# Optimization experiments

Hardware: AMD Instinct MI355X
Metric: run time of the kernel (lower is better)

## Reference

```python
import jax, jax.numpy as jnp
from jax import lax
import numpy as np

GRIDS = [40, 36, 24, 16, 12]
STRIDES = [4, 8, 16, 32, 64]
SCORE_THR = 0.3
MASK_THR = 0.5
UPDATE_THR = 0.05
SIGMA = 2.0
NMS_PRE = 500
MAX_PER_IMG = 30
E = 128            # ins_out_channels -> kernel_out_channels
HF = WF = 128      # seg feature map; upsampled_size_out = 4*HF = 512
IMG_H = IMG_W = 512
ORI_H = ORI_W = 512

# per-candidate stride, matching the cumsum-based fill in get_seg_single
STRIDE_PER_CELL = np.repeat(np.array(STRIDES, np.float32), [g * g for g in GRIDS])  # [3872]


def setup_inputs() -> dict:
    key = jax.random.key(0)
    ks = jax.random.split(key, 11)
    d = {}
    for i, g in enumerate(GRIDS):
        d[f"cate{i}"] = jax.random.uniform(ks[i], (1, g, g, 1), jnp.float32)
        d[f"kern{i}"] = jax.random.normal(ks[5 + i], (1, E, g, g), jnp.float32)
    d["seg_pred"] = jax.random.normal(ks[10], (1, E, HF, WF), jnp.float32)
    return d


def _forward_scores_and_masks(cates, kerns, seg_pred):
    # flatten all FPN levels, exactly mirroring view(-1,C)/permute(1,2,0).view(-1,E)
    scores = jnp.concatenate([c[0].reshape(-1) for c in cates])                 # [M]
    kernels = jnp.concatenate([k[0].transpose(1, 2, 0).reshape(-1, E) for k in kerns])  # [M,E]
    strides = jnp.asarray(STRIDE_PER_CELL)
    valid = scores > SCORE_THR                                                  # score_thr filter (as mask)

    # dynamic 1x1 conv over mask features == channel contraction
    seg_preds = jax.nn.sigmoid(jnp.einsum('me,ehw->mhw', kernels, seg_pred[0]))  # [M,HF,WF]
    seg_masks = seg_preds > MASK_THR
    sum_masks = seg_masks.sum((1, 2)).astype(jnp.float32)
    keep = valid & (sum_masks > strides)
    seg_scores = (seg_preds * seg_masks).sum((1, 2)) / jnp.maximum(sum_masks, 1.0)
    cscores = jnp.where(keep, scores * seg_scores, 0.0)

    # descending sort + truncate to nms_pre (dropped candidates carry score 0)
    top_scores, top_idx = lax.top_k(cscores, NMS_PRE)
    masks_k = seg_masks[top_idx].reshape(NMS_PRE, -1).astype(jnp.float32)       # [N,HW]
    sm = sum_masks[top_idx]

    # matrix NMS (single foreground class -> label matrix = triu of ones)
    inter = masks_k @ masks_k.T                                                 # [N,N]
    union = sm[None, :] + sm[:, None] - inter
    iou = jnp.triu(inter / jnp.maximum(union, 1.0), k=1)
    comp = iou.max(0)                              # max IoU with any higher-scored mask
    decay = jnp.exp(-SIGMA * (iou ** 2 - comp[:, None] ** 2))
    decay_coeff = decay.min(0)
    nms_scores = top_scores * decay_coeff
    nms_scores = jnp.where(nms_scores >= UPDATE_THR, nms_scores, 0.0)           # update_thr filter

    final_scores, fidx = lax.top_k(nms_scores, MAX_PER_IMG)
    sel = top_idx[fidx]
    sel_preds = seg_preds[sel]                                                  # [K,HF,WF]
    up = jax.image.resize(sel_preds, (MAX_PER_IMG, HF * 4, WF * 4), 'bilinear')  # align_corners=False
    up = up[:, :IMG_H, :IMG_W]
    up = jax.image.resize(up, (MAX_PER_IMG, ORI_H, ORI_W), 'bilinear')
    return final_scores, up


def reference(cate0, cate1, cate2, cate3, cate4,
              kern0, kern1, kern2, kern3, kern4, seg_pred):
    cates = [cate0, cate1, cate2, cate3, cate4]
    kerns = [kern0, kern1, kern2, kern3, kern4]
    final_scores, up = _forward_scores_and_masks(cates, kerns, seg_pred)
    seg_label = up > MASK_THR                                                   # [K,H,W]
    vis = final_scores > SCORE_THR                                              # vis_inds in forward()

    # masks_to_boxes, vectorized; invalid/empty rows zeroed (fixed-size output)
    any_x = seg_label.any(1)                                                    # [K,W]
    any_y = seg_label.any(2)                                                    # [K,H]
    xs = jnp.arange(ORI_W)
    ys = jnp.arange(ORI_H)
    xmin = jnp.min(jnp.where(any_x, xs, ORI_W), axis=1)
    xmax = jnp.max(jnp.where(any_x, xs, -1), axis=1)
    ymin = jnp.min(jnp.where(any_y, ys, ORI_H), axis=1)
    ymax = jnp.max(jnp.where(any_y, ys, -1), axis=1)
    boxes = jnp.stack([xmin, ymin, xmax, ymax], -1).astype(jnp.float32)         # [K,4]
    boxes = jnp.where(vis[:, None], boxes, 0.0)
    return boxes, final_scores, vis.astype(jnp.float32)
```

## Files before the change

kernel.cpp:

```cpp
#include <hip/hip_runtime.h>
#include <math.h>

#define M_CELLS 3872
#define M_PAD   3968
#define NPIX    16384

typedef _Float16 half8 __attribute__((ext_vector_type(8)));
typedef float f32x4 __attribute__((ext_vector_type(4)));

#define GL2LDS(g, l) __builtin_amdgcn_global_load_lds( \
    (const __attribute__((address_space(1))) unsigned int*)(g), \
    (__attribute__((address_space(3))) unsigned int*)(l), 16, 0, 0)

static constexpr size_t ALN(size_t x){ return (x + 255) & ~(size_t)255; }

static constexpr size_t F_KF   = 0;
static constexpr size_t F_SC   = F_KF + (size_t)M_CELLS*128*4;
static constexpr size_t F_SM   = F_SC + (size_t)M_CELLS*4;
static constexpr size_t F_CS   = F_SM + (size_t)M_CELLS*4;
static constexpr size_t F_BIT  = F_CS + (size_t)M_CELLS*4;
static constexpr size_t F_SPP  = F_BIT + (size_t)M_CELLS*256*8;
static constexpr size_t F_TIDX = F_SPP + (size_t)64*M_CELLS*4;
static constexpr size_t F_TSC  = F_TIDX + 512*4;
static constexpr size_t F_SMT  = F_TSC + 512*4;
static constexpr size_t F_IOU  = F_SMT + 512*4;
static constexpr size_t F_COMP = F_IOU + (size_t)500*500*4;
static constexpr size_t F_NMS  = F_COMP + 512*4;
static constexpr size_t F_SEL  = F_NMS + 512*4;
static constexpr size_t F_SELP = F_SEL + 32*4;
static constexpr size_t F_GAX  = ALN(F_SELP + (size_t)30*NPIX*4);
static constexpr size_t F_GAY  = F_GAX + 30*512*4;
static constexpr size_t F_KEYS = ALN(F_GAY + 30*512*4);
static constexpr size_t WS_FB  = F_KEYS + 4096*8;

static constexpr size_t B_KF   = 0;
static constexpr size_t B_AFR  = ALN(B_KF  + (size_t)M_PAD*128*4);
static constexpr size_t B_BFR  = ALN(B_AFR + (size_t)31*4096*16);
static constexpr size_t B_SC   = ALN(B_BFR + (size_t)128*4096*16);
static constexpr size_t B_SM   = ALN(B_SC + (size_t)M_PAD*4);
static constexpr size_t B_CS   = ALN(B_SM + (size_t)M_PAD*4);
static constexpr size_t B_BIT  = ALN(B_CS + (size_t)M_PAD*4);
static constexpr size_t B_SPP  = ALN(B_BIT + (size_t)M_PAD*256*8);
static constexpr size_t B_TIDX = ALN(B_SPP + (size_t)128*M_PAD*4);
static constexpr size_t B_TSC  = ALN(B_TIDX + 512*4);
static constexpr size_t B_SMT  = ALN(B_TSC + 512*4);
static constexpr size_t B_IOU  = ALN(B_SMT + 512*4);
static constexpr size_t B_COMP = ALN(B_IOU + (size_t)500*500*4);
static constexpr size_t B_NMS  = ALN(B_COMP + 512*4);
static constexpr size_t B_SEL  = ALN(B_NMS + 512*4);
static constexpr size_t B_SELP = ALN(B_SEL + 32*4);
static constexpr size_t B_GAX  = ALN(B_SELP + (size_t)30*NPIX*4);
static constexpr size_t B_GAY  = B_GAX + 30*512*4;
static constexpr size_t B_CMAP = ALN(B_GAY + 30*512*4);
static constexpr size_t B_RMAP = B_CMAP + 4096*4;
static constexpr size_t B_VCNT = B_RMAP + 4096*4;
static constexpr size_t B_KEYS = ALN(B_VCNT + 64*4);
static constexpr size_t B_AF30 = ALN(B_KEYS + 4096*8);
static constexpr size_t WS_MFMA = B_AF30 + 8*128*16;

__global__ __launch_bounds__(256) void k0a_gather(
    const float* __restrict__ c0,const float* __restrict__ c1,const float* __restrict__ c2,
    const float* __restrict__ c3,const float* __restrict__ c4,
    const float* __restrict__ w0,const float* __restrict__ w1,const float* __restrict__ w2,
    const float* __restrict__ w3,const float* __restrict__ w4,
    float* __restrict__ kf, float* __restrict__ scores) {
  const int lvl = blockIdx.y;
  const int Gs[5]   = {1600,1296,576,256,144};
  const int offs[5] = {0,1600,2896,3472,3728};
  const int G = Gs[lvl], off = offs[lvl];
  const float* kl = (lvl==0)?w0:(lvl==1)?w1:(lvl==2)?w2:(lvl==3)?w3:w4;
  const float* cl = (lvl==0)?c0:(lvl==1)?c1:(lvl==2)?c2:(lvl==3)?c3:c4;
  int t = blockIdx.x*256 + threadIdx.x;
  if (t >= G*128) return;
  int e = t / G, c = t - e*G;
  kf[(size_t)(off+c)*128 + e] = kl[t];
  if (e == 0) scores[off+c] = cl[c];
}

__global__ __launch_bounds__(1024) void k_compact(const float* __restrict__ scores,
                                                  int* __restrict__ cmap, int* __restrict__ rmap,
                                                  int* __restrict__ vcnt) {
  __shared__ int tsum[1024];
  int tid = threadIdx.x;
  int base = tid*4;
  int f[4]; int s = 0;
  #pragma unroll
  for (int j=0;j<4;j++) {
    int c = base+j;
    f[j] = (c < M_CELLS && scores[c] > 0.3f) ? 1 : 0;
    s += f[j];
  }
  tsum[tid] = s;
  __syncthreads();
  for (int off=1; off<1024; off<<=1) {
    int v = (tid >= off) ? tsum[tid-off] : 0;
    __syncthreads();
    tsum[tid] += v;
    __syncthreads();
  }
  int run = tsum[tid] - s;
  #pragma unroll
  for (int j=0;j<4;j++) {
    int c = base+j;
    if (c < M_CELLS) {
      if (f[j]) { cmap[run] = c; rmap[c] = run; run++; }
      else rmap[c] = -1;
    }
  }
  if (tid == 1023) vcnt[0] = tsum[1023];
}

__global__ __launch_bounds__(256) void k0b_afrag(const float* __restrict__ kf,
                                                 const int* __restrict__ cmap,
                                                 const int* __restrict__ vcnt,
                                                 _Float16* __restrict__ Af) {
  int P = blockIdx.x*256 + threadIdx.x;
  int mblock = P >> 12;
  int r  = P & 4095;
  int sub = r >> 9, pc = r & 511;
  int ks = sub >> 1, h = sub & 1;
  int mn = pc >> 6, ln = pc & 63;
  int mcomp = mblock*128 + mn*16 + (ln & 15);
  int kb = ks*32 + (ln >> 4)*8;
  half8 o;
  if (mcomp < vcnt[0]) {
    const float* src = kf + (size_t)cmap[mcomp]*128 + kb;
    #pragma unroll
    for (int j=0;j<8;j++) {
      float x = src[j];
      _Float16 hi = (_Float16)x;
      o[j] = h ? (_Float16)(x - (float)hi) : hi;
    }
  } else {
    #pragma unroll
    for (int j=0;j<8;j++) o[j] = (_Float16)0.f;
  }
  *(half8*)&Af[(size_t)P*8] = o;
}

__global__ __launch_bounds__(256) void k0c_bfrag(const float* __restrict__ seg,
                                                 _Float16* __restrict__ Bf) {
  int P = blockIdx.x*256 + threadIdx.x;
  int nb = P >> 12;
  int r  = P & 4095;
  int sub = r >> 9, pc = r & 511;
  int ks = sub >> 1, h = sub & 1;
  int mn = pc >> 6, ln = pc & 63;
  int px = nb*128 + mn*16 + (ln & 15);
  int kb = ks*32 + (ln >> 4)*8;
  half8 o;
  #pragma unroll
  for (int j=0;j<8;j++) {
    float x = seg[(size_t)(kb+j)*NPIX + px];
    _Float16 hi = (_Float16)x;
    o[j] = h ? (_Float16)(x - (float)hi) : hi;
  }
  *(half8*)&Bf[(size_t)P*8] = o;
}

__global__ __launch_bounds__(256, 6) void k1_gemm(
    const float* __restrict__ kf, const float* __restrict__ seg,
    unsigned long long* __restrict__ bits, float* __restrict__ spp) {
  int tid = threadIdx.x;
  int p  = blockIdx.x*256 + tid;
  int c0 = blockIdx.y*32;
  float acc[32];
  #pragma unroll
  for (int c=0;c<32;c++) acc[c]=0.f;
  for (int ch=0; ch<8; ch++) {
    float s[16];
    #pragma unroll
    for (int e=0;e<16;e++) s[e] = seg[(size_t)(ch*16+e)*NPIX + p];
    #pragma unroll
    for (int c=0;c<32;c++) {
      float a=0.f;
      #pragma unroll
      for (int e=0;e<16;e++) a = fmaf(kf[(size_t)(c0+c)*128 + ch*16 + e], s[e], a);
      acc[c] += a;
    }
  }
  int wv = tid>>6, ln = tid&63;
  __shared__ float wsum[32][4];
  #pragma unroll
  for (int c=0;c<32;c++) {
    float logit = acc[c];
    bool msk = logit > 0.f;
    unsigned long long bal = __ballot(msk);
    float pr = msk ? __fdividef(1.f, 1.f + __expf(-logit)) : 0.f;
    #pragma unroll
    for (int o=32;o>0;o>>=1) pr += __shfl_down(pr, o);
    if (ln==0) {
      bits[(size_t)(c0+c)*256 + blockIdx.x*4 + wv] = bal;
      wsum[c][wv] = pr;
    }
  }
  __syncthreads();
  if (tid < 32)
    spp[(size_t)blockIdx.x*M_CELLS + c0 + tid] = wsum[tid][0]+wsum[tid][1]+wsum[tid][2]+wsum[tid][3];
}

__global__ __launch_bounds__(256, 4) void k1_mfma(
    const _Float16* __restrict__ Af, const _Float16* __restrict__ Bf,
    const int* __restrict__ vcnt,
    unsigned long long* __restrict__ bits, float* __restrict__ spp) {
  if (blockIdx.x*128 >= vcnt[0]) return;
  __shared__ char lds[32768];
  const int tid  = threadIdx.x;
  const int lane = tid & 63;
  const int wave = tid >> 6;
  const int wr = wave >> 1, wc = wave & 1;
  const char* gA = (const char*)Af + (size_t)blockIdx.x*65536;
  const char* gB = (const char*)Bf + (size_t)blockIdx.y*65536;

  f32x4 acc[4][4];
  #pragma unroll
  for (int a=0;a<4;a++)
    #pragma unroll
    for (int b=0;b<4;b++) acc[a][b] = (f32x4){0.f,0.f,0.f,0.f};

  auto issue = [&](int sub, int buf) {
    const char* ga = gA + sub*8192;
    const char* gb = gB + sub*8192;
    char* la = &lds[buf*16384];
    char* lb = &lds[buf*16384 + 8192];
    GL2LDS(ga +  wave   *1024 + lane*16, la +  wave   *1024);
    GL2LDS(ga + (wave+4)*1024 + lane*16, la + (wave+4)*1024);
    GL2LDS(gb +  wave   *1024 + lane*16, lb +  wave   *1024);
    GL2LDS(gb + (wave+4)*1024 + lane*16, lb + (wave+4)*1024);
  };

  issue(0, 0);
  half8 ah[4], bh[4];
  #pragma unroll
  for (int s=0; s<8; s++) {
    __syncthreads();
    if (s < 7) issue(s+1, (s+1)&1);
    const char* lb_ = &lds[(s&1)*16384];
    if ((s & 1) == 0) {
      #pragma unroll
      for (int mt=0; mt<4; mt++) ah[mt] = *(const half8*)&lb_[(wr*4+mt)*1024 + lane*16];
      #pragma unroll
      for (int nt=0; nt<4; nt++) bh[nt] = *(const half8*)&lb_[8192 + (wc*4+nt)*1024 + lane*16];
      #pragma unroll
      for (int nt=0; nt<4; nt++)
        #pragma unroll
        for (int mt=0; mt<4; mt++)
          acc[mt][nt] = __builtin_amdgcn_mfma_f32_16x16x32_f16(ah[mt], bh[nt], acc[mt][nt], 0, 0, 0);
    } else {
      #pragma unroll
      for (int nt=0; nt<4; nt++) {
        half8 bl = *(const half8*)&lb_[8192 + (wc*4+nt)*1024 + lane*16];
        #pragma unroll
        for (int mt=0; mt<4; mt++)
          acc[mt][nt] = __builtin_amdgcn_mfma_f32_16x16x32_f16(ah[mt], bl, acc[mt][nt], 0, 0, 0);
      }
      #pragma unroll
      for (int mt=0; mt<4; mt++) {
        half8 al = *(const half8*)&lb_[(wr*4+mt)*1024 + lane*16];
        #pragma unroll
        for (int nt=0; nt<4; nt++)
          acc[mt][nt] = __builtin_amdgcn_mfma_f32_16x16x32_f16(al, bh[nt], acc[mt][nt], 0, 0, 0);
      }
    }
  }
  __syncthreads();

  const int q = lane >> 4, mm = lane & 15;
  const int mbase = blockIdx.x * 128;
  const int wordIdx = blockIdx.y*2 + wc;
  float* ldsf = (float*)lds;
  #pragma unroll
  for (int mt=0; mt<4; mt++) {
    #pragma unroll
    for (int reg=0; reg<4; reg++) {
      unsigned long long bal[4];
      float ps = 0.f;
      #pragma unroll
      for (int nt=0; nt<4; nt++) {
        float lg = acc[mt][nt][reg];
        bal[nt] = __ballot(lg > 0.f);
        if (lg > 0.f) ps += __fdividef(1.f, 1.f + __expf(-lg));
      }
      ps += __shfl_xor(ps, 1); ps += __shfl_xor(ps, 2);
      ps += __shfl_xor(ps, 4); ps += __shfl_xor(ps, 8);
      if (mm == 0) {
        int cl = wr*64 + mt*16 + q*4 + reg;
        unsigned long long wd = 0;
        #pragma unroll
        for (int nt=0; nt<4; nt++)
          wd |= ((bal[nt] >> (q*16)) & 0xFFFFull) << (nt*16);
        bits[(size_t)(mbase + cl)*256 + wordIdx] = wd;
        ldsf[cl*2 + wc] = ps;
      }
    }
  }
  __syncthreads();
  if (tid < 128)
    spp[(size_t)blockIdx.y*M_PAD + mbase + tid] = ldsf[tid*2] + ldsf[tid*2+1];
}

__global__ __launch_bounds__(256) void k2c_cscore(
    const unsigned long long* __restrict__ bits, const float* __restrict__ spp,
    const float* __restrict__ scores, const int* __restrict__ rmap,
    float* __restrict__ summ, float* __restrict__ cs) {
  int cell = blockIdx.x*4 + (threadIdx.x>>6);
  int ln = threadIdx.x & 63;
  int ridx = rmap[cell];
  if (ridx < 0) { if (ln==0) { summ[cell]=0.f; cs[cell]=0.f; } return; }
  const unsigned long long* row = bits + (size_t)ridx*256;
  int cnt = 0;
  #pragma unroll
  for (int k=0;k<4;k++) cnt += __popcll(row[ln + 64*k]);
  float sp = 0.f;
  for (int i=ln; i<128; i+=64) sp += spp[(size_t)i*M_PAD + ridx];
  #pragma unroll
  for (int o=32;o>0;o>>=1) { cnt += __shfl_down(cnt,o); sp += __shfl_down(sp,o); }
  if (ln==0) {
    float smf = (float)cnt;
    float sc = scores[cell];
    float strd = (cell<1600)?4.f:(cell<2896)?8.f:(cell<3472)?16.f:(cell<3728)?32.f:64.f;
    bool keep = (smf > strd);
    float ss = sp / fmaxf(smf, 1.f);
    summ[cell] = smf;
    cs[cell] = keep ? sc*ss : 0.f;
  }
}

__global__ __launch_bounds__(256) void k2_cscore(
    const unsigned long long* __restrict__ bits, const float* __restrict__ spp,
    const float* __restrict__ scores, float* __restrict__ summ, float* __restrict__ cs,
    int nparts, int mp) {
  int cell = blockIdx.x*4 + (threadIdx.x>>6);
  int ln = threadIdx.x & 63;
  const unsigned long long* row = bits + (size_t)cell*256;
  int cnt = 0;
  #pragma unroll
  for (int k=0;k<4;k++) cnt += __popcll(row[ln + 64*k]);
  float sp = 0.f;
  for (int i=ln; i<nparts; i+=64) sp += spp[(size_t)i*mp + cell];
  #pragma unroll
  for (int o=32;o>0;o>>=1) { cnt += __shfl_down(cnt,o); sp += __shfl_down(sp,o); }
  if (ln==0) {
    float smf = (float)cnt;
    float sc = scores[cell];
    float strd = (cell<1600)?4.f:(cell<2896)?8.f:(cell<3472)?16.f:(cell<3728)?32.f:64.f;
    bool keep = (sc > 0.3f) && (smf > strd);
    float ss = sp / fmaxf(smf, 1.f);
    summ[cell] = smf;
    cs[cell] = keep ? sc*ss : 0.f;
  }
}

__device__ inline unsigned long long packkey(float v, int i) {
  return ((unsigned long long)__float_as_uint(v) << 32) | (unsigned)(0xFFFFFFFFu - (unsigned)i);
}

__global__ __launch_bounds__(256) void k3a_sort512(const float* __restrict__ cs,
                                                   unsigned long long* __restrict__ keys) {
  __shared__ unsigned long long key[512];
  int b = blockIdx.x, tid = threadIdx.x;
  for (int i=tid;i<512;i+=256) {
    int gi = b*512 + i;
    key[i] = (gi < M_CELLS) ? packkey(cs[gi], gi) : 0ULL;
  }
  __syncthreads();
  for (int size=2; size<=512; size<<=1) {
    for (int st=size>>1; st>0; st>>=1) {
      for (int i=tid;i<512;i+=256) {
        int pp = i ^ st;
        if (pp > i) {
          unsigned long long a=key[i], bb=key[pp];
          bool desc = (((b*512+i) & size) == 0);
          if (desc ? (a<bb) : (a>bb)) { key[i]=bb; key[pp]=a; }
        }
      }
      __syncthreads();
    }
  }
  for (int i=tid;i<512;i+=256) keys[b*512+i] = key[i];
}

__global__ __launch_bounds__(1024) void k3b_merge(const unsigned long long* __restrict__ keys,
    const float* __restrict__ summ,
    int* __restrict__ tidx, float* __restrict__ tsc, float* __restrict__ smt) {
  __shared__ unsigned long long key[4096];
  int tid = threadIdx.x;
  for (int i=tid;i<4096;i+=1024) key[i] = keys[i];
  __syncthreads();
  for (int size=1024; size<=4096; size<<=1) {
    for (int st=size>>1; st>0; st>>=1) {
      for (int i=tid;i<4096;i+=1024) {
        int pp = i ^ st;
        if (pp > i) {
          unsigned long long a=key[i], b=key[pp];
          bool desc = ((i & size) == 0);
          if (desc ? (a<b) : (a>b)) { key[i]=b; key[pp]=a; }
        }
      }
      __syncthreads();
    }
  }
  if (tid < 512) {
    if (tid < 500) {
      unsigned long long k = key[tid];
      int idx = (int)(0xFFFFFFFFu - (unsigned)(k & 0xFFFFFFFFull));
      tidx[tid] = idx;
      tsc[tid] = __uint_as_float((unsigned)(k>>32));
      smt[tid] = summ[idx];
    } else { tidx[tid]=0; tsc[tid]=0.f; smt[tid]=0.f; }
  }
}

__global__ __launch_bounds__(256) void k4_iou(
    const unsigned long long* __restrict__ bits, const int* __restrict__ tidx,
    const int* __restrict__ rmap, const float* __restrict__ smt, float* __restrict__ iou) {
  int ti = blockIdx.y, tj = blockIdx.x;
  int tid = threadIdx.x;
  int ty = tid>>4, tx = tid&15;
  int i = ti*16+ty, j = tj*16+tx;
  if (ti > tj) { if (i<500 && j<500) iou[i*500+j] = 0.f; return; }
  __shared__ unsigned long long A[16][130];
  __shared__ unsigned long long B[16][130];
  __shared__ float sa[16], sb[16];
  if (tid<16) sa[tid] = (ti*16+tid<500) ? smt[ti*16+tid] : 0.f;
  else if (tid<32) sb[tid-16] = (tj*16+tid-16<500) ? smt[tj*16+tid-16] : 0.f;
  int inter = 0;
  for (int half=0; half<2; half++) {
    __syncthreads();
    for (int t=tid;t<2048;t+=256) {
      int r=t>>7, k=t&127;
      int ii = ti*16+r;
      int jj = tj*16+r;
      int ri = (ii<500) ? (rmap ? max(rmap[tidx[ii]],0) : tidx[ii]) : 0;
      int rj = (jj<500) ? (rmap ? max(rmap[tidx[jj]],0) : tidx[jj]) : 0;
      A[r][k] = (ii<500) ? bits[(size_t)ri*256 + half*128 + k] : 0ULL;
      B[r][k] = (jj<500) ? bits[(size_t)rj*256 + half*128 + k] : 0ULL;
    }
    __syncthreads();
    for (int k=0;k<128;k++) inter += __popcll(A[ty][k] & B[tx][k]);
  }
  if (i<500 && j<500) {
    float fi = (float)inter;
    float un = sa[ty] + sb[tx] - fi;
    iou[i*500+j] = (i<j) ? fi / fmaxf(un, 1.f) : 0.f;
  }
}

__global__ __launch_bounds__(256) void k5_comp(const float* __restrict__ iou, float* __restrict__ comp) {
  int tid = threadIdx.x;
  int tx = tid & 63, ty = tid >> 6;
  int j = blockIdx.x*64 + tx;
  float m0=0.f, m1=0.f, m2=0.f, m3=0.f;
  if (j < 500) {
    int i = ty;
    for (; i+12 < 500; i += 16) {
      m0 = fmaxf(m0, iou[(i   )*500 + j]);
      m1 = fmaxf(m1, iou[(i+ 4)*500 + j]);
      m2 = fmaxf(m2, iou[(i+ 8)*500 + j]);
      m3 = fmaxf(m3, iou[(i+12)*500 + j]);
    }
    for (; i < 500; i += 4) m0 = fmaxf(m0, iou[i*500 + j]);
  }
  float m = fmaxf(fmaxf(m0,m1), fmaxf(m2,m3));
  __shared__ float red[4][64];
  red[ty][tx] = m;
  __syncthreads();
  if (ty == 0 && j < 512)
    comp[j] = (j < 500) ? fmaxf(fmaxf(red[0][tx],red[1][tx]), fmaxf(red[2][tx],red[3][tx])) : 0.f;
}

__global__ __launch_bounds__(256) void k6_decay(
    const float* __restrict__ iou, const float* __restrict__ comp,
    const float* __restrict__ tsc, float* __restrict__ nms) {
  __shared__ float csh[512];
  int tid = threadIdx.x;
  for (int i=tid; i<512; i+=256) csh[i] = (i<500) ? comp[i] : 0.f;
  __syncthreads();
  int tx = tid & 63, ty = tid >> 6;
  int j = blockIdx.x*64 + tx;
  float t0=-1e30f, t1=-1e30f, t2=-1e30f, t3=-1e30f;
  if (j < 500) {
    int i = ty;
    for (; i+12 < 500; i += 16) {
      float v0 = iou[(i   )*500 + j], c0 = csh[i];
      float v1 = iou[(i+ 4)*500 + j], c1 = csh[i+4];
      float v2 = iou[(i+ 8)*500 + j], c2 = csh[i+8];
      float v3 = iou[(i+12)*500 + j], c3 = csh[i+12];
      t0 = fmaxf(t0, v0*v0 - c0*c0);
      t1 = fmaxf(t1, v1*v1 - c1*c1);
      t2 = fmaxf(t2, v2*v2 - c2*c2);
      t3 = fmaxf(t3, v3*v3 - c3*c3);
    }
    for (; i < 500; i += 4) { float v = iou[i*500 + j]; float c = csh[i]; t0 = fmaxf(t0, v*v - c*c); }
  }
  float t = fmaxf(fmaxf(t0,t1), fmaxf(t2,t3));
  __shared__ float red[4][64];
  red[ty][tx] = t;
  __syncthreads();
  if (ty == 0 && j < 512) {
    float out = 0.f;
    if (j < 500) {
      float tt = fmaxf(fmaxf(red[0][tx],red[1][tx]), fmaxf(red[2][tx],red[3][tx]));
      float s = tsc[j] * __expf(-2.f*tt);
      out = (s >= 0.05f) ? s : 0.f;
    }
    nms[j] = out;
  }
}

__global__ __launch_bounds__(256) void k7_top30(
    const float* __restrict__ nms, const int* __restrict__ tidx,
    int* __restrict__ sel, float* __restrict__ out) {
  __shared__ unsigned long long key[512];
  int tid = threadIdx.x;
  for (int i=tid;i<512;i+=256) key[i] = (i<500) ? packkey(nms[i], i) : 0ULL;
  __syncthreads();
  for (int size=2; size<=512; size<<=1) {
    for (int st=size>>1; st>0; st>>=1) {
      for (int i=tid;i<512;i+=256) {
        int pp = i ^ st;
        if (pp > i) {
          unsigned long long a=key[i], b=key[pp];
          bool desc = ((i & size) == 0);
          if (desc ? (a<b) : (a>b)) { key[i]=b; key[pp]=a; }
        }
      }
      __syncthreads();
    }
  }
  if (tid < 30) {
    unsigned long long k = key[tid];
    int j = (int)(0xFFFFFFFFu - (unsigned)(k & 0xFFFFFFFFull));
    float v = __uint_as_float((unsigned)(k>>32));
    out[120+tid] = v;
    out[150+tid] = (v > 0.3f) ? 1.f : 0.f;
    sel[tid] = tidx[j];
  }
}

__global__ __launch_bounds__(256) void k7b_af30(const float* __restrict__ kf,
                                                const int* __restrict__ sel,
                                                _Float16* __restrict__ Af30) {
  for (int P = threadIdx.x; P < 1024; P += 256) {
    int sub = P >> 7, pc = P & 127;
    int ks = sub >> 1, h = sub & 1;
    int mn = pc >> 6, ln = pc & 63;
    int m  = mn*16 + (ln & 15);
    int kb = ks*32 + (ln >> 4)*8;
    half8 o;
    if (m < 30) {
      const float* src = kf + (size_t)sel[m]*128 + kb;
      #pragma unroll
      for (int j=0;j<8;j++) {
        float x = src[j];
        _Float16 hi = (_Float16)x;
        o[j] = h ? (_Float16)(x - (float)hi) : hi;
      }
    } else {
      #pragma unroll
      for (int j=0;j<8;j++) o[j] = (_Float16)0.f;
    }
    *(half8*)&Af30[(size_t)P*8] = o;
  }
}

__global__ __launch_bounds__(256) void k8_mfma(const _Float16* __restrict__ Af30,
                                               const _Float16* __restrict__ Bf,
                                               float* __restrict__ selp) {
  const int nb = blockIdx.x;
  const int lane = threadIdx.x & 63;
  const int w = threadIdx.x >> 6;
  const half8* A = (const half8*)Af30;
  const half8* B = (const half8*)Bf + (size_t)nb*4096;
  f32x4 acc[2][2];
  #pragma unroll
  for (int a=0;a<2;a++)
    #pragma unroll
    for (int b=0;b<2;b++) acc[a][b] = (f32x4){0.f,0.f,0.f,0.f};
  #pragma unroll
  for (int ks=0; ks<4; ks++) {
    half8 ah[2], bh[2], al[2], bl[2];
    #pragma unroll
    for (int mt=0; mt<2; mt++) ah[mt] = A[(ks*2+0)*128 + mt*64 + lane];
    #pragma unroll
    for (int nt=0; nt<2; nt++) bh[nt] = B[(size_t)(ks*2+0)*512 + (w*2+nt)*64 + lane];
    #pragma unroll
    for (int mt=0; mt<2; mt++) al[mt] = A[(ks*2+1)*128 + mt*64 + lane];
    #pragma unroll
    for (int nt=0; nt<2; nt++) bl[nt] = B[(size_t)(ks*2+1)*512 + (w*2+nt)*64 + lane];
    #pragma unroll
    for (int nt=0; nt<2; nt++)
      #pragma unroll
      for (int mt=0; mt<2; mt++) {
        acc[mt][nt] = __builtin_amdgcn_mfma_f32_16x16x32_f16(ah[mt], bh[nt], acc[mt][nt], 0, 0, 0);
        acc[mt][nt] = __builtin_amdgcn_mfma_f32_16x16x32_f16(ah[mt], bl[nt], acc[mt][nt], 0, 0, 0);
        acc[mt][nt] = __builtin_amdgcn_mfma_f32_16x16x32_f16(al[mt], bh[nt], acc[mt][nt], 0, 0, 0);
      }
  }
  const int q = lane >> 4, col = lane & 15;
  #pragma unroll
  for (int mt=0; mt<2; mt++)
    #pragma unroll
    for (int nt=0; nt<2; nt++)
      #pragma unroll
      for (int reg=0; reg<4; reg++) {
        int m = mt*16 + q*4 + reg;
        if (m < 30) {
          int px = nb*128 + w*32 + nt*16 + col;
          float lg = acc[mt][nt][reg];
          selp[(size_t)m*NPIX + px] = __fdividef(1.f, 1.f + __expf(-lg));
        }
      }
}

__global__ __launch_bounds__(256) void k8_selp(
    const float* __restrict__ kf, const float* __restrict__ seg,
    const int* __restrict__ sel, float* __restrict__ selp) {
  int px = blockIdx.x*256 + threadIdx.x;
  int cells[30];
  #pragma unroll
  for (int m=0;m<30;m++) cells[m] = __builtin_amdgcn_readfirstlane(sel[m]);
  float acc[30];
  #pragma unroll
  for (int m=0;m<30;m++) acc[m] = 0.f;
  for (int e=0; e<128; e+=4) {
    float s0 = seg[(size_t)(e+0)*NPIX + px];
    float s1 = seg[(size_t)(e+1)*NPIX + px];
    float s2 = seg[(size_t)(e+2)*NPIX + px];
    float s3 = seg[(size_t)(e+3)*NPIX + px];
    #pragma unroll
    for (int m=0;m<30;m++) {
      const float* kr = kf + (size_t)cells[m]*128 + e;
      acc[m] = fmaf(kr[0], s0, fmaf(kr[1], s1, fmaf(kr[2], s2, fmaf(kr[3], s3, acc[m]))));
    }
  }
  #pragma unroll
  for (int m=0;m<30;m++)
    selp[(size_t)m*NPIX + px] = __fdividef(1.f, 1.f + __expf(-acc[m]));
}

__global__ __launch_bounds__(256) void k9a_rows(const float* __restrict__ selp,
                                               int* __restrict__ gax, int* __restrict__ gay) {
  int msk = blockIdx.y, oy = blockIdx.x;
  const float* mp = selp + (size_t)msk*NPIX;
  __shared__ float rows[2][128];
  int tid = threadIdx.x;
  float yf = fminf(fmaxf((oy+0.5f)*0.25f - 0.5f, 0.f), 127.f);
  int y0 = (int)yf, y1 = min(y0+1,127);
  float fy = yf-(float)y0;
  if (tid < 128) rows[0][tid] = mp[y0*128 + tid];
  else           rows[1][tid-128] = mp[y1*128 + tid-128];
  __syncthreads();
  int occ = 0;
  #pragma unroll
  for (int h=0; h<2; h++) {
    int ox = tid + h*256;
    float xf = fminf(fmaxf((ox+0.5f)*0.25f - 0.5f, 0.f), 127.f);
    int x0 = (int)xf, x1 = min(x0+1,127);
    float fx = xf-(float)x0;
    float v0 = rows[0][x0]*(1.f-fx) + rows[0][x1]*fx;
    float v1 = rows[1][x0]*(1.f-fx) + rows[1][x1]*fx;
    float v  = v0*(1.f-fy) + v1*fy;
    if (v > 0.5f) { gax[msk*512 + ox] = 1; occ = 1; }
  }
  if (__syncthreads_or(occ)) { if (tid == 0) gay[msk*512 + oy] = 1; }
}

__global__ __launch_bounds__(512) void k9b_box(const int* __restrict__ gax,
                                              const int* __restrict__ gay, float* out) {
  int msk = blockIdx.x, tid = threadIdx.x;
  __shared__ int r0[512], r1[512], r2[512], r3[512];
  int ax = gax[msk*512 + tid], ay = gay[msk*512 + tid];
  r0[tid] = ax ? tid : 512;
  r1[tid] = ax ? tid : -1;
  r2[tid] = ay ? tid : 512;
  r3[tid] = ay ? tid : -1;
  __syncthreads();
  for (int s=256;s>0;s>>=1) {
    if (tid<s) {
      r0[tid]=min(r0[tid],r0[tid+s]); r1[tid]=max(r1[tid],r1[tid+s]);
      r2[tid]=min(r2[tid],r2[tid+s]); r3[tid]=max(r3[tid],r3[tid+s]);
    }
    __syncthreads();
  }
  if (tid==0) {
    bool vis = out[120+msk] > 0.3f;
    out[msk*4+0] = vis ? (float)r0[0] : 0.f;
    out[msk*4+1] = vis ? (float)r2[0] : 0.f;
    out[msk*4+2] = vis ? (float)r1[0] : 0.f;
    out[msk*4+3] = vis ? (float)r3[0] : 0.f;
  }
}

extern "C" void kernel_launch(void* const* d_in, const int* in_sizes, int n_in,
                              void* d_out, int out_size, void* d_ws, size_t ws_size,
                              hipStream_t stream) {
  (void)in_sizes; (void)n_in; (void)out_size;
  if (ws_size < WS_FB) return;
  const float* cate[5]; const float* kern[5];
  for (int i=0;i<5;i++){ cate[i]=(const float*)d_in[2*i]; kern[i]=(const float*)d_in[2*i+1]; }
  const float* seg = (const float*)d_in[10];
  char* ws = (char*)d_ws;
  float* out = (float*)d_out;

  const bool mfma = (ws_size >= WS_MFMA);

  float* kf      = (float*)(ws + (mfma ? B_KF   : F_KF));
  float* scores  = (float*)(ws + (mfma ? B_SC   : F_SC));
  float* summ    = (float*)(ws + (mfma ? B_SM   : F_SM));
  float* cs      = (float*)(ws + (mfma ? B_CS   : F_CS));
  unsigned long long* bits = (unsigned long long*)(ws + (mfma ? B_BIT : F_BIT));
  float* spp     = (float*)(ws + (mfma ? B_SPP  : F_SPP));
  int*   tidx    = (int*)(ws + (mfma ? B_TIDX : F_TIDX));
  float* tsc     = (float*)(ws + (mfma ? B_TSC  : F_TSC));
  float* smt     = (float*)(ws + (mfma ? B_SMT  : F_SMT));
  float* iou     = (float*)(ws + (mfma ? B_IOU  : F_IOU));
  float* comp    = (float*)(ws + (mfma ? B_COMP : F_COMP));
  float* nms     = (float*)(ws + (mfma ? B_NMS  : F_NMS));
  int*   sel     = (int*)(ws + (mfma ? B_SEL  : F_SEL));
  float* selp    = (float*)(ws + (mfma ? B_SELP : F_SELP));
  int*   gax     = (int*)(ws + (mfma ? B_GAX  : F_GAX));
  int*   gay     = (int*)(ws + (mfma ? B_GAY  : F_GAY));
  unsigned long long* keys = (unsigned long long*)(ws + (mfma ? B_KEYS : F_KEYS));

  hipMemsetAsync(gax, 0, 30*512*4*2, stream);

  k0a_gather<<<dim3(800,5), 256, 0, stream>>>(cate[0],cate[1],cate[2],cate[3],cate[4],
                                    kern[0],kern[1],kern[2],kern[3],kern[4], kf, scores);
  const int* rmap_for_k4 = nullptr;
  if (mfma) {
    _Float16* Af = (_Float16*)(ws + B_AFR);
    _Float16* Bf = (_Float16*)(ws + B_BFR);
    _Float16* Af30 = (_Float16*)(ws + B_AF30);
    int* cmap = (int*)(ws + B_CMAP);
    int* rmap = (int*)(ws + B_RMAP);
    int* vcnt = (int*)(ws + B_VCNT);
    rmap_for_k4 = rmap;
    k_compact<<<1, 1024, 0, stream>>>(scores, cmap, rmap, vcnt);
    k0b_afrag<<<31*4096/256, 256, 0, stream>>>(kf, cmap, vcnt, Af);
    k0c_bfrag<<<128*4096/256, 256, 0, stream>>>(seg, Bf);
    k1_mfma  <<<dim3(31, 128), 256, 0, stream>>>(Af, Bf, vcnt, bits, spp);
    k2c_cscore<<<M_CELLS/4, 256, 0, stream>>>(bits, spp, scores, rmap, summ, cs);
    k3a_sort512<<<8, 256, 0, stream>>>(cs, keys);
    k3b_merge  <<<1, 1024, 0, stream>>>(keys, summ, tidx, tsc, smt);
    k4_iou   <<<dim3(32,32), 256, 0, stream>>>(bits, tidx, rmap_for_k4, smt, iou);
    k5_comp  <<<8, 256, 0, stream>>>(iou, comp);
    k6_decay <<<8, 256, 0, stream>>>(iou, comp, tsc, nms);
    k7_top30 <<<1, 256, 0, stream>>>(nms, tidx, sel, out);
    k7b_af30 <<<1, 256, 0, stream>>>(kf, sel, Af30);
    k8_mfma  <<<128, 256, 0, stream>>>(Af30, Bf, selp);
  } else {
    k1_gemm  <<<dim3(64,121), 256, 0, stream>>>(kf, seg, bits, spp);
    k2_cscore<<<M_CELLS/4, 256, 0, stream>>>(bits, spp, scores, summ, cs, 64, M_CELLS);
    k3a_sort512<<<8, 256, 0, stream>>>(cs, keys);
    k3b_merge  <<<1, 1024, 0, stream>>>(keys, summ, tidx, tsc, smt);
    k4_iou   <<<dim3(32,32), 256, 0, stream>>>(bits, tidx, nullptr, smt, iou);
    k5_comp  <<<8, 256, 0, stream>>>(iou, comp);
    k6_decay <<<8, 256, 0, stream>>>(iou, comp, tsc, nms);
    k7_top30 <<<1, 256, 0, stream>>>(nms, tidx, sel, out);
    k8_selp  <<<NPIX/256, 256, 0, stream>>>(kf, seg, sel, selp);
  }
  k9a_rows <<<dim3(512,30), 256, 0, stream>>>(selp, gax, gay);
  k9b_box  <<<30, 512, 0, stream>>>(gax, gay, out);
}
```

Baseline: 292.6 us.

## Fuse compaction into transposed gather, fold af30 into top30, atomic box reduction

```diff
diff --git a/kernel.cpp b/kernel.cpp
--- a/kernel.cpp
+++ b/kernel.cpp
@@ -28,9 +28,8 @@
 static constexpr size_t F_NMS  = F_COMP + 512*4;
 static constexpr size_t F_SEL  = F_NMS + 512*4;
 static constexpr size_t F_SELP = F_SEL + 32*4;
-static constexpr size_t F_GAX  = ALN(F_SELP + (size_t)30*NPIX*4);
-static constexpr size_t F_GAY  = F_GAX + 30*512*4;
-static constexpr size_t F_KEYS = ALN(F_GAY + 30*512*4);
+static constexpr size_t F_BOX  = ALN(F_SELP + (size_t)30*NPIX*4);
+static constexpr size_t F_KEYS = ALN(F_BOX + 128*4);
 static constexpr size_t WS_FB  = F_KEYS + 4096*8;
 
 static constexpr size_t B_KF   = 0;
@@ -49,14 +48,42 @@
 static constexpr size_t B_NMS  = ALN(B_COMP + 512*4);
 static constexpr size_t B_SEL  = ALN(B_NMS + 512*4);
 static constexpr size_t B_SELP = ALN(B_SEL + 32*4);
-static constexpr size_t B_GAX  = ALN(B_SELP + (size_t)30*NPIX*4);
-static constexpr size_t B_GAY  = B_GAX + 30*512*4;
-static constexpr size_t B_CMAP = ALN(B_GAY + 30*512*4);
+static constexpr size_t B_BOX  = ALN(B_SELP + (size_t)30*NPIX*4);
+static constexpr size_t B_CMAP = ALN(B_BOX + 128*4);
 static constexpr size_t B_RMAP = B_CMAP + 4096*4;
 static constexpr size_t B_VCNT = B_RMAP + 4096*4;
 static constexpr size_t B_KEYS = ALN(B_VCNT + 64*4);
 static constexpr size_t B_AF30 = ALN(B_KEYS + 4096*8);
 static constexpr size_t WS_MFMA = B_AF30 + 8*128*16;
+
+__global__ __launch_bounds__(256) void k0aT_gather(
+    const float* __restrict__ c0,const float* __restrict__ c1,const float* __restrict__ c2,
+    const float* __restrict__ c3,const float* __restrict__ c4,
+    const float* __restrict__ w0,const float* __restrict__ w1,const float* __restrict__ w2,
+    const float* __restrict__ w3,const float* __restrict__ w4,
+    float* __restrict__ kfT, float* __restrict__ scores,
+    int* __restrict__ cmap, int* __restrict__ rmap, int* __restrict__ vcnt) {
+  const int lvl = blockIdx.y;
+  const int Gs[5]   = {1600,1296,576,256,144};
+  const int offs[5] = {0,1600,2896,3472,3728};
+  const int G = Gs[lvl], off = offs[lvl];
+  const float* kl = (lvl==0)?w0:(lvl==1)?w1:(lvl==2)?w2:(lvl==3)?w3:w4;
+  const float* cl = (lvl==0)?c0:(lvl==1)?c1:(lvl==2)?c2:(lvl==3)?c3:c4;
+  int t = blockIdx.x*256 + threadIdx.x;
+  if (t >= G*128) return;
+  int e = t / G, c = t - e*G;
+  kfT[(size_t)e*M_PAD + off + c] = kl[t];
+  if (e == 0) {
+    int cell = off + c;
+    float sc = cl[c];
+    scores[cell] = sc;
+    if (sc > 0.3f) {
+      int run = atomicAdd(vcnt, 1);
+      cmap[run] = cell;
+      rmap[cell] = run;
+    } else rmap[cell] = -1;
+  }
+}
 
 __global__ __launch_bounds__(256) void k0a_gather(
     const float* __restrict__ c0,const float* __restrict__ c1,const float* __restrict__ c2,
@@ -77,40 +104,7 @@
   if (e == 0) scores[off+c] = cl[c];
 }
 
-__global__ __launch_bounds__(1024) void k_compact(const float* __restrict__ scores,
-                                                  int* __restrict__ cmap, int* __restrict__ rmap,
-                                                  int* __restrict__ vcnt) {
-  __shared__ int tsum[1024];
-  int tid = threadIdx.x;
-  int base = tid*4;
-  int f[4]; int s = 0;
-  #pragma unroll
-  for (int j=0;j<4;j++) {
-    int c = base+j;
-    f[j] = (c < M_CELLS && scores[c] > 0.3f) ? 1 : 0;
-    s += f[j];
-  }
-  tsum[tid] = s;
-  __syncthreads();
-  for (int off=1; off<1024; off<<=1) {
-    int v = (tid >= off) ? tsum[tid-off] : 0;
-    __syncthreads();
-    tsum[tid] += v;
-    __syncthreads();
-  }
-  int run = tsum[tid] - s;
-  #pragma unroll
-  for (int j=0;j<4;j++) {
-    int c = base+j;
-    if (c < M_CELLS) {
-      if (f[j]) { cmap[run] = c; rmap[c] = run; run++; }
-      else rmap[c] = -1;
-    }
-  }
-  if (tid == 1023) vcnt[0] = tsum[1023];
-}
-
-__global__ __launch_bounds__(256) void k0b_afrag(const float* __restrict__ kf,
+__global__ __launch_bounds__(256) void k0b_afrag(const float* __restrict__ kfT,
                                                  const int* __restrict__ cmap,
                                                  const int* __restrict__ vcnt,
                                                  _Float16* __restrict__ Af) {
@@ -124,10 +118,10 @@
   int kb = ks*32 + (ln >> 4)*8;
   half8 o;
   if (mcomp < vcnt[0]) {
-    const float* src = kf + (size_t)cmap[mcomp]*128 + kb;
+    const float* src = kfT + cmap[mcomp];
     #pragma unroll
     for (int j=0;j<8;j++) {
-      float x = src[j];
+      float x = src[(size_t)(kb+j)*M_PAD];
       _Float16 hi = (_Float16)x;
       o[j] = h ? (_Float16)(x - (float)hi) : hi;
     }
@@ -510,8 +504,10 @@
 
 __global__ __launch_bounds__(256) void k7_top30(
     const float* __restrict__ nms, const int* __restrict__ tidx,
-    int* __restrict__ sel, float* __restrict__ out) {
+    int* __restrict__ sel, float* __restrict__ out,
+    const float* __restrict__ kfT, _Float16* __restrict__ Af30) {
   __shared__ unsigned long long key[512];
+  __shared__ int selsh[30];
   int tid = threadIdx.x;
   for (int i=tid;i<512;i+=256) key[i] = (i<500) ? packkey(nms[i], i) : 0ULL;
   __syncthreads();
@@ -535,32 +531,31 @@
     out[120+tid] = v;
     out[150+tid] = (v > 0.3f) ? 1.f : 0.f;
     sel[tid] = tidx[j];
-  }
-}
-
-__global__ __launch_bounds__(256) void k7b_af30(const float* __restrict__ kf,
-                                                const int* __restrict__ sel,
-                                                _Float16* __restrict__ Af30) {
-  for (int P = threadIdx.x; P < 1024; P += 256) {
-    int sub = P >> 7, pc = P & 127;
-    int ks = sub >> 1, h = sub & 1;
-    int mn = pc >> 6, ln = pc & 63;
-    int m  = mn*16 + (ln & 15);
-    int kb = ks*32 + (ln >> 4)*8;
-    half8 o;
-    if (m < 30) {
-      const float* src = kf + (size_t)sel[m]*128 + kb;
-      #pragma unroll
-      for (int j=0;j<8;j++) {
-        float x = src[j];
-        _Float16 hi = (_Float16)x;
-        o[j] = h ? (_Float16)(x - (float)hi) : hi;
-      }
-    } else {
-      #pragma unroll
-      for (int j=0;j<8;j++) o[j] = (_Float16)0.f;
-    }
-    *(half8*)&Af30[(size_t)P*8] = o;
+    selsh[tid] = tidx[j];
+  }
+  __syncthreads();
+  if (kfT) {
+    for (int P = tid; P < 1024; P += 256) {
+      int sub = P >> 7, pc = P & 127;
+      int ks = sub >> 1, h = sub & 1;
+      int mn = pc >> 6, ln = pc & 63;
+      int m  = mn*16 + (ln & 15);
+      int kb = ks*32 + (ln >> 4)*8;
+      half8 o;
+      if (m < 30) {
+        const float* src = kfT + selsh[m];
+        #pragma unroll
+        for (int j=0;j<8;j++) {
+          float x = src[(size_t)(kb+j)*M_PAD];
+          _Float16 hi = (_Float16)x;
+          o[j] = h ? (_Float16)(x - (float)hi) : hi;
+        }
+      } else {
+        #pragma unroll
+        for (int j=0;j<8;j++) o[j] = (_Float16)0.f;
+      }
+      *(half8*)&Af30[(size_t)P*8] = o;
+    }
   }
 }
 
@@ -640,10 +635,11 @@
 }
 
 __global__ __launch_bounds__(256) void k9a_rows(const float* __restrict__ selp,
-                                               int* __restrict__ gax, int* __restrict__ gay) {
+                                               int* __restrict__ box) {
   int msk = blockIdx.y, oy = blockIdx.x;
   const float* mp = selp + (size_t)msk*NPIX;
   __shared__ float rows[2][128];
+  __shared__ int wmn[4], wmx[4];
   int tid = threadIdx.x;
   float yf = fminf(fmaxf((oy+0.5f)*0.25f - 0.5f, 0.f), 127.f);
   int y0 = (int)yf, y1 = min(y0+1,127);
@@ -651,7 +647,7 @@
   if (tid < 128) rows[0][tid] = mp[y0*128 + tid];
   else           rows[1][tid-128] = mp[y1*128 + tid-128];
   __syncthreads();
-  int occ = 0;
+  int mnx = 512, mxx = -1;
   #pragma unroll
   for (int h=0; h<2; h++) {
     int ox = tid + h*256;
@@ -661,35 +657,39 @@
     float v0 = rows[0][x0]*(1.f-fx) + rows[0][x1]*fx;
     float v1 = rows[1][x0]*(1.f-fx) + rows[1][x1]*fx;
     float v  = v0*(1.f-fy) + v1*fy;
-    if (v > 0.5f) { gax[msk*512 + ox] = 1; occ = 1; }
-  }
-  if (__syncthreads_or(occ)) { if (tid == 0) gay[msk*512 + oy] = 1; }
-}
-
-__global__ __launch_bounds__(512) void k9b_box(const int* __restrict__ gax,
-                                              const int* __restrict__ gay, float* out) {
-  int msk = blockIdx.x, tid = threadIdx.x;
-  __shared__ int r0[512], r1[512], r2[512], r3[512];
-  int ax = gax[msk*512 + tid], ay = gay[msk*512 + tid];
-  r0[tid] = ax ? tid : 512;
-  r1[tid] = ax ? tid : -1;
-  r2[tid] = ay ? tid : 512;
-  r3[tid] = ay ? tid : -1;
-  __syncthreads();
-  for (int s=256;s>0;s>>=1) {
-    if (tid<s) {
-      r0[tid]=min(r0[tid],r0[tid+s]); r1[tid]=max(r1[tid],r1[tid+s]);
-      r2[tid]=min(r2[tid],r2[tid+s]); r3[tid]=max(r3[tid],r3[tid+s]);
-    }
-    __syncthreads();
-  }
-  if (tid==0) {
-    bool vis = out[120+msk] > 0.3f;
-    out[msk*4+0] = vis ? (float)r0[0] : 0.f;
-    out[msk*4+1] = vis ? (float)r2[0] : 0.f;
-    out[msk*4+2] = vis ? (float)r1[0] : 0.f;
-    out[msk*4+3] = vis ? (float)r3[0] : 0.f;
-  }
+    if (v > 0.5f) { mnx = min(mnx, ox); mxx = max(mxx, ox); }
+  }
+  #pragma unroll
+  for (int o=32;o>0;o>>=1) {
+    mnx = min(mnx, __shfl_down(mnx, o));
+    mxx = max(mxx, __shfl_down(mxx, o));
+  }
+  if ((tid & 63) == 0) { wmn[tid>>6] = mnx; wmx[tid>>6] = mxx; }
+  __syncthreads();
+  if (tid == 0) {
+    int a = min(min(wmn[0],wmn[1]), min(wmn[2],wmn[3]));
+    int b = max(max(wmx[0],wmx[1]), max(wmx[2],wmx[3]));
+    if (b >= 0) {
+      atomicMin(&box[msk],      a);
+      atomicMin(&box[32 + msk], oy);
+      atomicMax(&box[64 + msk], b);
+      atomicMax(&box[96 + msk], oy);
+    }
+  }
+}
+
+__global__ __launch_bounds__(64) void k9b_box(const int* __restrict__ box, float* out) {
+  int m = threadIdx.x;
+  if (m >= 30) return;
+  bool vis = out[120+m] > 0.3f;
+  int xmn = min(box[m], 512);
+  int ymn = min(box[32+m], 512);
+  int xmx = box[64+m];
+  int ymx = box[96+m];
+  out[m*4+0] = vis ? (float)xmn : 0.f;
+  out[m*4+1] = vis ? (float)ymn : 0.f;
+  out[m*4+2] = vis ? (float)xmx : 0.f;
+  out[m*4+3] = vis ? (float)ymx : 0.f;
 }
 
 extern "C" void kernel_launch(void* const* d_in, const int* in_sizes, int n_in,
@@ -719,15 +719,12 @@
   float* nms     = (float*)(ws + (mfma ? B_NMS  : F_NMS));
   int*   sel     = (int*)(ws + (mfma ? B_SEL  : F_SEL));
   float* selp    = (float*)(ws + (mfma ? B_SELP : F_SELP));
-  int*   gax     = (int*)(ws + (mfma ? B_GAX  : F_GAX));
-  int*   gay     = (int*)(ws + (mfma ? B_GAY  : F_GAY));
+  int*   box     = (int*)(ws + (mfma ? B_BOX  : F_BOX));
   unsigned long long* keys = (unsigned long long*)(ws + (mfma ? B_KEYS : F_KEYS));
 
-  hipMemsetAsync(gax, 0, 30*512*4*2, stream);
-
-  k0a_gather<<<dim3(800,5), 256, 0, stream>>>(cate[0],cate[1],cate[2],cate[3],cate[4],
-                                    kern[0],kern[1],kern[2],kern[3],kern[4], kf, scores);
-  const int* rmap_for_k4 = nullptr;
+  hipMemsetAsync(box,      0x7F, 64*4, stream);
+  hipMemsetAsync(box + 64, 0xFF, 64*4, stream);
+
   if (mfma) {
     _Float16* Af = (_Float16*)(ws + B_AFR);
     _Float16* Bf = (_Float16*)(ws + B_BFR);
@@ -735,21 +732,24 @@
     int* cmap = (int*)(ws + B_CMAP);
     int* rmap = (int*)(ws + B_RMAP);
     int* vcnt = (int*)(ws + B_VCNT);
-    rmap_for_k4 = rmap;
-    k_compact<<<1, 1024, 0, stream>>>(scores, cmap, rmap, vcnt);
+    hipMemsetAsync(vcnt, 0, 4, stream);
+    k0aT_gather<<<dim3(800,5), 256, 0, stream>>>(cate[0],cate[1],cate[2],cate[3],cate[4],
+                                      kern[0],kern[1],kern[2],kern[3],kern[4],
+                                      kf, scores, cmap, rmap, vcnt);
+    k0c_bfrag<<<128*4096/256, 256, 0, stream>>>(seg, Bf);
     k0b_afrag<<<31*4096/256, 256, 0, stream>>>(kf, cmap, vcnt, Af);
-    k0c_bfrag<<<128*4096/256, 256, 0, stream>>>(seg, Bf);
     k1_mfma  <<<dim3(31, 128), 256, 0, stream>>>(Af, Bf, vcnt, bits, spp);
     k2c_cscore<<<M_CELLS/4, 256, 0, stream>>>(bits, spp, scores, rmap, summ, cs);
     k3a_sort512<<<8, 256, 0, stream>>>(cs, keys);
     k3b_merge  <<<1, 1024, 0, stream>>>(keys, summ, tidx, tsc, smt);
-    k4_iou   <<<dim3(32,32), 256, 0, stream>>>(bits, tidx, rmap_for_k4, smt, iou);
+    k4_iou   <<<dim3(32,32), 256, 0, stream>>>(bits, tidx, rmap, smt, iou);
     k5_comp  <<<8, 256, 0, stream>>>(iou, comp);
     k6_decay <<<8, 256, 0, stream>>>(iou, comp, tsc, nms);
-    k7_top30 <<<1, 256, 0, stream>>>(nms, tidx, sel, out);
-    k7b_af30 <<<1, 256, 0, stream>>>(kf, sel, Af30);
+    k7_top30 <<<1, 256, 0, stream>>>(nms, tidx, sel, out, kf, Af30);
     k8_mfma  <<<128, 256, 0, stream>>>(Af30, Bf, selp);
   } else {
+    k0a_gather<<<dim3(800,5), 256, 0, stream>>>(cate[0],cate[1],cate[2],cate[3],cate[4],
+                                      kern[0],kern[1],kern[2],kern[3],kern[4], kf, scores);
     k1_gemm  <<<dim3(64,121), 256, 0, stream>>>(kf, seg, bits, spp);
     k2_cscore<<<M_CELLS/4, 256, 0, stream>>>(bits, spp, scores, summ, cs, 64, M_CELLS);
     k3a_sort512<<<8, 256, 0, stream>>>(cs, keys);
@@ -757,9 +757,9 @@
     k4_iou   <<<dim3(32,32), 256, 0, stream>>>(bits, tidx, nullptr, smt, iou);
     k5_comp  <<<8, 256, 0, stream>>>(iou, comp);
     k6_decay <<<8, 256, 0, stream>>>(iou, comp, tsc, nms);
-    k7_top30 <<<1, 256, 0, stream>>>(nms, tidx, sel, out);
+    k7_top30 <<<1, 256, 0, stream>>>(nms, tidx, sel, out, nullptr, nullptr);
     k8_selp  <<<NPIX/256, 256, 0, stream>>>(kf, seg, sel, selp);
   }
-  k9a_rows <<<dim3(512,30), 256, 0, stream>>>(selp, gax, gay);
-  k9b_box  <<<30, 512, 0, stream>>>(gax, gay, out);
-}
+  k9a_rows <<<dim3(512,30), 256, 0, stream>>>(selp, box);
+  k9b_box  <<<1, 64, 0, stream>>>(box, out);
+}
```

Result: slower. 434.3 us (+48.5%).
